# Kernel tuning notes

Hardware: AMD Instinct MI355X
Metric: run time of the kernel (lower is better)

## Reference

```python
import jax, jax.numpy as jnp
import numpy as np

DQ, DM = 1024, 512  # dim_query, dim_mem


def setup_inputs() -> dict:
    key = jax.random.key(0)
    k1, k2, k3, k4, k5, k6 = jax.random.split(key, 6)
    B, S, M = 4, 2048, 4096
    x = jax.random.normal(k1, (B, S, DQ), dtype=jnp.float32)
    memory = jax.random.normal(k2, (B, M, DM), dtype=jnp.float32)
    # nn.Linear params: weight [out, in], bias [out]
    Wq = jax.random.normal(k3, (DM, DQ), dtype=jnp.float32) / np.sqrt(DQ)
    bq = jax.random.normal(k4, (DM,), dtype=jnp.float32) * 0.01
    Wm = jax.random.normal(k5, (DQ, DM), dtype=jnp.float32) / np.sqrt(DM)
    bm = jax.random.normal(k6, (DQ,), dtype=jnp.float32) * 0.01
    return {"x": x, "memory": memory, "Wq": Wq, "bq": bq, "Wm": Wm, "bm": bm}


def reference(x, memory, Wq, bq, Wm, bm):
    # query_transform: [B,S,DQ] -> [B,S,DM]
    query = jnp.einsum('bsq,mq->bsm', x, Wq) + bq
    # unscaled single-head cross-attention over memory slots
    scores = jnp.einsum('bsd,bmd->bsm', query, memory)  # [B,S,M]
    weights = jax.nn.softmax(scores, axis=-1)
    attended = jnp.einsum('bsm,bmd->bsd', weights, memory)  # [B,S,DM]
    # memory_transform: [B,S,DM] -> [B,S,DQ]
    transformed = jnp.einsum('bsd,qd->bsq', attended, Wm) + bm
    return (x, transformed)
```

## Files before the change

kernel.cpp:

```cpp
#include <hip/hip_runtime.h>

typedef unsigned short u16;
typedef __bf16 bf16x8 __attribute__((ext_vector_type(8)));
typedef float f32x4 __attribute__((ext_vector_type(4)));
typedef unsigned short u16x8 __attribute__((ext_vector_type(8)));
typedef unsigned short u16x4 __attribute__((ext_vector_type(4)));

__device__ __forceinline__ u16 f2bf(float f) {
    unsigned u = __builtin_bit_cast(unsigned, f);
    u += 0x7FFFu + ((u >> 16) & 1u);
    return (u16)(u >> 16);
}
__device__ __forceinline__ float bf2f(u16 s) {
    return __builtin_bit_cast(float, ((unsigned)s) << 16);
}

__device__ __forceinline__ void gload16(u16* lds, const u16* g) {
    __builtin_amdgcn_global_load_lds(
        (__attribute__((address_space(1))) unsigned*)g,
        (__attribute__((address_space(3))) unsigned*)lds,
        16, 0, 0);
}

__device__ __forceinline__ void remap_xy(int xcx, int& bx, int& by) {
    const int nx = gridDim.x;
    const int d = blockIdx.y * nx + blockIdx.x;
    const int xcd = d & 7, i = d >> 3;
    const int xcy = 8 / xcx;
    const int cw = nx / xcx;
    const int ch = (int)gridDim.y / xcy;
    bx = (xcd % xcx) * cw + i % cw;
    by = (xcd / xcx) * ch + i / cw;
}

#define BM 128
#define BN 128
#define BK 32
#define TILE (BM * BK)
#define BK2 64
#define TILE2 (BM * BK2)

__device__ __forceinline__ void stage_tile(u16* lds, const u16* src, long long ld,
                                           int k0, int wave, int lane)
{
#pragma unroll
    for (int i = 0; i < 2; ++i) {
        const int segb = wave * 64 + i * 256;
        const int seg  = segb + lane;
        const int r  = seg >> 2;
        const int qs = seg & 3;
        const int qg = qs ^ ((r >> 1) & 3);
        gload16(lds + segb * 8, src + (long long)r * ld + k0 + qg * 8);
    }
}
__device__ __forceinline__ bf16x8 frag(const u16* lds, int row, int quad) {
    const int slot = quad ^ ((row >> 1) & 3);
    return __builtin_bit_cast(bf16x8, *(const u16x8*)(lds + row * BK + slot * 8));
}

__device__ __forceinline__ void stage_tile64(u16* lds, const u16* src, long long ld,
                                             int k0, int wave, int lane)
{
#pragma unroll
    for (int i = 0; i < 4; ++i) {
        const int segb = wave * 64 + i * 256;
        const int seg  = segb + lane;
        const int r  = seg >> 3;
        const int qs = seg & 7;
        const int qg = qs ^ (r & 7);
        gload16(lds + segb * 8, src + (long long)r * ld + k0 + qg * 8);
    }
}
__device__ __forceinline__ bf16x8 frag64(const u16* lds, int row, int quad, int kw) {
    const int slot = (kw * 4 + quad) ^ (row & 7);
    return __builtin_bit_cast(bf16x8, *(const u16x8*)(lds + row * BK2 + slot * 8));
}

#define WAIT8_BARRIER()  asm volatile("s_waitcnt vmcnt(8)\n\ts_barrier" ::: "memory")
#define WAIT0_BARRIER()  asm volatile("s_waitcnt vmcnt(0)\n\ts_barrier" ::: "memory")
#define BARRIER()        asm volatile("s_barrier" ::: "memory")

template<bool SPLITOUT>
__global__ void gemm_cat3(const u16* __restrict__ Ah, const u16* __restrict__ Al,
                          const u16* __restrict__ Bh, const u16* __restrict__ Bl,
                          const float* __restrict__ bias,
                          void* __restrict__ C, u16* __restrict__ Cl,
                          int K, long long lda, long long ldb, long long ldc,
                          int xcx)
{
    __shared__ u16 sm[2][4][TILE];
    const int t = threadIdx.x;
    const int wave = t >> 6, lane = t & 63, quad = lane >> 4, l16 = lane & 15;
    const int waveM = (wave & 1) * 64, waveN = (wave >> 1) * 64;
    int bx, by;
    remap_xy(xcx, bx, by);
    const long long rowBase = (long long)by * BM;
    const long long colBase = (long long)bx * BN;
    Ah += rowBase * lda; Al += rowBase * lda;
    Bh += colBase * ldb; Bl += colBase * ldb;

    f32x4 acc[4][4];
#pragma unroll
    for (int i = 0; i < 4; ++i)
#pragma unroll
        for (int j = 0; j < 4; ++j) acc[i][j] = (f32x4){0.f, 0.f, 0.f, 0.f};

    auto stage4 = [&](int buf, int k0) {
        stage_tile(sm[buf][0], Ah, lda, k0, wave, lane);
        stage_tile(sm[buf][1], Al, lda, k0, wave, lane);
        stage_tile(sm[buf][2], Bh, ldb, k0, wave, lane);
        stage_tile(sm[buf][3], Bl, ldb, k0, wave, lane);
    };

    stage4(0, 0);
    int cur = 0;
    for (int k0 = 0; k0 < K; k0 += BK) {
        if (k0 + BK < K) {
            stage4(cur ^ 1, k0 + BK);
            WAIT8_BARRIER();
        } else {
            WAIT0_BARRIER();
        }

        bf16x8 ah[4], al[4], bh[4], bl[4];
#pragma unroll
        for (int mi = 0; mi < 4; ++mi) {
            int row = waveM + mi * 16 + l16;
            ah[mi] = frag(sm[cur][0], row, quad);
            al[mi] = frag(sm[cur][1], row, quad);
        }
#pragma unroll
        for (int ni = 0; ni < 4; ++ni) {
            int row = waveN + ni * 16 + l16;
            bh[ni] = frag(sm[cur][2], row, quad);
            bl[ni] = frag(sm[cur][3], row, quad);
        }
#pragma unroll
        for (int mi = 0; mi < 4; ++mi)
#pragma unroll
            for (int ni = 0; ni < 4; ++ni) {
                acc[mi][ni] = __builtin_amdgcn_mfma_f32_16x16x32_bf16(al[mi], bh[ni], acc[mi][ni], 0, 0, 0);
                acc[mi][ni] = __builtin_amdgcn_mfma_f32_16x16x32_bf16(ah[mi], bl[ni], acc[mi][ni], 0, 0, 0);
                acc[mi][ni] = __builtin_amdgcn_mfma_f32_16x16x32_bf16(ah[mi], bh[ni], acc[mi][ni], 0, 0, 0);
            }

        BARRIER();
        cur ^= 1;
    }

#pragma unroll
    for (int mi = 0; mi < 4; ++mi) {
#pragma unroll
        for (int ni = 0; ni < 4; ++ni) {
            long long col = colBase + waveN + ni * 16 + l16;
            float bv = bias ? bias[col] : 0.0f;
#pragma unroll
            for (int r = 0; r < 4; ++r) {
                long long row = rowBase + waveM + mi * 16 + quad * 4 + r;
                float f = acc[mi][ni][r] + bv;
                long long off = row * ldc + col;
                if (SPLITOUT) {
                    u16 h = f2bf(f);
                    ((u16*)C)[off] = h;
                    Cl[off] = f2bf(f - bf2f(h));
                } else {
                    ((float*)C)[off] = f;
                }
            }
        }
    }
}

template<bool OUTF32>
__global__ void gemm_bf(const u16* __restrict__ A, const u16* __restrict__ B,
                        const float* __restrict__ bias, void* __restrict__ C,
                        int K, long long lda, long long ldb, long long ldc,
                        int xcx)
{
    __shared__ u16 sm[2][2][TILE2];
    const int t = threadIdx.x;
    const int wave = t >> 6, lane = t & 63, quad = lane >> 4, l16 = lane & 15;
    const int waveM = (wave & 1) * 64, waveN = (wave >> 1) * 64;
    int bx, by;
    remap_xy(xcx, bx, by);
    const long long rowBase = (long long)by * BM;
    const long long colBase = (long long)bx * BN;
    A += rowBase * lda;
    B += colBase * ldb;

    f32x4 acc[4][4];
#pragma unroll
    for (int i = 0; i < 4; ++i)
#pragma unroll
        for (int j = 0; j < 4; ++j) acc[i][j] = (f32x4){0.f, 0.f, 0.f, 0.f};

    auto stage2 = [&](int buf, int k0) {
        stage_tile64(sm[buf][0], A, lda, k0, wave, lane);
        stage_tile64(sm[buf][1], B, ldb, k0, wave, lane);
    };

    stage2(0, 0);
    int cur = 0;
    for (int k0 = 0; k0 < K; k0 += BK2) {
        if (k0 + BK2 < K) {
            stage2(cur ^ 1, k0 + BK2);
            WAIT8_BARRIER();
        } else {
            WAIT0_BARRIER();
        }

#pragma unroll
        for (int kw = 0; kw < 2; ++kw) {
            bf16x8 af[4], bfr[4];
#pragma unroll
            for (int mi = 0; mi < 4; ++mi) af[mi]  = frag64(sm[cur][0], waveM + mi * 16 + l16, quad, kw);
#pragma unroll
            for (int ni = 0; ni < 4; ++ni) bfr[ni] = frag64(sm[cur][1], waveN + ni * 16 + l16, quad, kw);
#pragma unroll
            for (int mi = 0; mi < 4; ++mi)
#pragma unroll
                for (int ni = 0; ni < 4; ++ni)
                    acc[mi][ni] = __builtin_amdgcn_mfma_f32_16x16x32_bf16(af[mi], bfr[ni], acc[mi][ni], 0, 0, 0);
        }

        BARRIER();
        cur ^= 1;
    }

#pragma unroll
    for (int mi = 0; mi < 4; ++mi) {
#pragma unroll
        for (int ni = 0; ni < 4; ++ni) {
            long long col = colBase + waveN + ni * 16 + l16;
            float bv = bias ? bias[col] : 0.0f;
#pragma unroll
            for (int r = 0; r < 4; ++r) {
                long long row = rowBase + waveM + mi * 16 + quad * 4 + r;
                float f = acc[mi][ni][r] + bv;
                long long off = row * ldc + col;
                if (OUTF32) ((float*)C)[off] = f;
                else        ((u16*)C)[off] = f2bf(f);
            }
        }
    }
}

__global__ void gemm_pv(const u16* __restrict__ A, const u16* __restrict__ B,
                        float* __restrict__ part, int KSEG,
                        long long lda, long long ldb)
{
    __shared__ u16 sm[2][2][TILE2];
    const int t = threadIdx.x;
    const int wave = t >> 6, lane = t & 63, quad = lane >> 4, l16 = lane & 15;
    const int waveM = (wave & 1) * 64, waveN = (wave >> 1) * 64;
    const int flat = (blockIdx.z * gridDim.y + blockIdx.y) * gridDim.x + blockIdx.x;
    const int xcd = flat & 7, i = flat >> 3;
    const int by = 2 * xcd + (i & 1);
    const int bx = (i >> 1) & 3;
    const int bz = i >> 3;
    const long long rowBase = (long long)by * BM;
    const long long colBase = (long long)bx * BN;
    const int kbase = bz * KSEG;
    A += rowBase * lda;
    B += colBase * ldb;

    f32x4 acc[4][4];
#pragma unroll
    for (int i2 = 0; i2 < 4; ++i2)
#pragma unroll
        for (int j = 0; j < 4; ++j) acc[i2][j] = (f32x4){0.f, 0.f, 0.f, 0.f};

    auto stage2 = [&](int buf, int k0) {
        stage_tile64(sm[buf][0], A, lda, k0, wave, lane);
        stage_tile64(sm[buf][1], B, ldb, k0, wave, lane);
    };

    stage2(0, kbase);
    int cur = 0;
    for (int k0 = kbase; k0 < kbase + KSEG; k0 += BK2) {
        if (k0 + BK2 < kbase + KSEG) {
            stage2(cur ^ 1, k0 + BK2);
            WAIT8_BARRIER();
        } else {
            WAIT0_BARRIER();
        }

#pragma unroll
        for (int kw = 0; kw < 2; ++kw) {
            bf16x8 af[4], bfr[4];
#pragma unroll
            for (int mi = 0; mi < 4; ++mi) af[mi]  = frag64(sm[cur][0], waveM + mi * 16 + l16, quad, kw);
#pragma unroll
            for (int ni = 0; ni < 4; ++ni) bfr[ni] = frag64(sm[cur][1], waveN + ni * 16 + l16, quad, kw);
#pragma unroll
            for (int mi = 0; mi < 4; ++mi)
#pragma unroll
                for (int ni = 0; ni < 4; ++ni)
                    acc[mi][ni] = __builtin_amdgcn_mfma_f32_16x16x32_bf16(af[mi], bfr[ni], acc[mi][ni], 0, 0, 0);
        }

        BARRIER();
        cur ^= 1;
    }

#pragma unroll
    for (int mi = 0; mi < 4; ++mi) {
#pragma unroll
        for (int ni = 0; ni < 4; ++ni) {
            long long col = colBase + waveN + ni * 16 + l16;
#pragma unroll
            for (int r = 0; r < 4; ++r) {
                long long row = rowBase + waveM + mi * 16 + quad * 4 + r;
                part[row * 4096 + 2048 + bz * 512 + col] = acc[mi][ni][r];
            }
        }
    }
}

__global__ void cvt_att(const float* __restrict__ Sc, u16* __restrict__ dst)
{
    const int row = blockIdx.x, t = threadIdx.x;
    const float* p = Sc + (long long)row * 4096 + 2048 + t * 4;
    float4 s0 = *(const float4*)(p);
    float4 s1 = *(const float4*)(p + 512);
    float4 s2 = *(const float4*)(p + 1024);
    float4 s3 = *(const float4*)(p + 1536);
    u16x4 v;
    v[0] = f2bf(s0.x + s1.x + s2.x + s3.x);
    v[1] = f2bf(s0.y + s1.y + s2.y + s3.y);
    v[2] = f2bf(s0.z + s1.z + s2.z + s3.z);
    v[3] = f2bf(s0.w + s1.w + s2.w + s3.w);
    *(u16x4*)(dst + (long long)row * 512 + t * 4) = v;
}

__global__ void split32(const float* __restrict__ src, u16* __restrict__ h,
                        u16* __restrict__ l, long long n)
{
    long long i = ((long long)blockIdx.x * blockDim.x + threadIdx.x) * 8;
    if (i >= n) return;
    float4 a = *(const float4*)(src + i);
    float4 b = *(const float4*)(src + i + 4);
    float v[8] = {a.x, a.y, a.z, a.w, b.x, b.y, b.z, b.w};
    u16x8 hv, lv;
#pragma unroll
    for (int j = 0; j < 8; ++j) {
        u16 hh = f2bf(v[j]);
        hv[j] = hh;
        lv[j] = f2bf(v[j] - bf2f(hh));
    }
    *(u16x8*)(h + i) = hv;
    *(u16x8*)(l + i) = lv;
}

__global__ void cvt32(const float* __restrict__ src, u16* __restrict__ dst, long long n)
{
    long long i = ((long long)blockIdx.x * blockDim.x + threadIdx.x) * 8;
    if (i >= n) return;
    float4 a = *(const float4*)(src + i);
    float4 b = *(const float4*)(src + i + 4);
    u16x8 v;
    v[0] = f2bf(a.x); v[1] = f2bf(a.y); v[2] = f2bf(a.z); v[3] = f2bf(a.w);
    v[4] = f2bf(b.x); v[5] = f2bf(b.y); v[6] = f2bf(b.z); v[7] = f2bf(b.w);
    *(u16x8*)(dst + i) = v;
}

__global__ void prep_mem(const float* __restrict__ src, u16* __restrict__ h,
                         u16* __restrict__ l, u16* __restrict__ tdst)
{
    __shared__ u16 tile[64][72];
    const int dBase = blockIdx.x * 64, mBase = blockIdx.y * 64;
    const int t = threadIdx.x;
#pragma unroll
    for (int i = 0; i < 4; ++i) {
        int seg = t + i * 256;
        int r = seg >> 4;
        int c = (seg & 15) << 2;
        long long off = (long long)(mBase + r) * 512 + dBase + c;
        float4 v = *(const float4*)(src + off);
        u16 h0 = f2bf(v.x), h1 = f2bf(v.y), h2 = f2bf(v.z), h3 = f2bf(v.w);
        tile[r][c] = h0; tile[r][c + 1] = h1; tile[r][c + 2] = h2; tile[r][c + 3] = h3;
        u16x4 hv; hv[0] = h0; hv[1] = h1; hv[2] = h2; hv[3] = h3;
        u16x4 lv;
        lv[0] = f2bf(v.x - bf2f(h0)); lv[1] = f2bf(v.y - bf2f(h1));
        lv[2] = f2bf(v.z - bf2f(h2)); lv[3] = f2bf(v.w - bf2f(h3));
        *(u16x4*)(h + off) = hv;
        *(u16x4*)(l + off) = lv;
    }
    __syncthreads();
#pragma unroll
    for (int i = 0; i < 2; ++i) {
        int seg = t + i * 256;
        int r = seg >> 3;
        int c = (seg & 7) << 3;
        u16x8 v;
#pragma unroll
        for (int j = 0; j < 8; ++j) v[j] = tile[c + j][r];
        *(u16x8*)(tdst + (long long)(dBase + r) * 4096 + mBase + c) = v;
    }
}

__global__ void softmax_rows(float* __restrict__ S)
{
    const int d = blockIdx.x;
    const int rowIdx = (d & 7) * 256 + (d >> 3);
    float* p = S + (long long)rowIdx * 4096;
    const int t = threadIdx.x;

    float4 v[4];
#pragma unroll
    for (int i = 0; i < 4; ++i) v[i] = ((const float4*)p)[t + i * 256];

    float m = -1e30f;
#pragma unroll
    for (int i = 0; i < 4; ++i)
        m = fmaxf(m, fmaxf(fmaxf(v[i].x, v[i].y), fmaxf(v[i].z, v[i].w)));
#pragma unroll
    for (int off = 32; off; off >>= 1) m = fmaxf(m, __shfl_xor(m, off));
    __shared__ float redm[4];
    if ((t & 63) == 0) redm[t >> 6] = m;
    __syncthreads();
    m = fmaxf(fmaxf(redm[0], redm[1]), fmaxf(redm[2], redm[3]));

    float s = 0.f;
#pragma unroll
    for (int i = 0; i < 4; ++i) {
        v[i].x = __expf(v[i].x - m); v[i].y = __expf(v[i].y - m);
        v[i].z = __expf(v[i].z - m); v[i].w = __expf(v[i].w - m);
        s += v[i].x + v[i].y + v[i].z + v[i].w;
    }
#pragma unroll
    for (int off = 32; off; off >>= 1) s += __shfl_xor(s, off);
    __shared__ float reds[4];
    if ((t & 63) == 0) reds[t >> 6] = s;
    __syncthreads();
    s = reds[0] + reds[1] + reds[2] + reds[3];
    const float inv = 1.0f / s;

    u16* pw = (u16*)p;
#pragma unroll
    for (int i = 0; i < 4; ++i) {
        u16x4 w;
        w[0] = f2bf(v[i].x * inv); w[1] = f2bf(v[i].y * inv);
        w[2] = f2bf(v[i].z * inv); w[3] = f2bf(v[i].w * inv);
        *(u16x4*)(pw + 4 * (t + i * 256)) = w;
    }
}

extern "C" void kernel_launch(void* const* d_in, const int* in_sizes, int n_in,
                              void* d_out, int out_size, void* d_ws, size_t ws_size,
                              hipStream_t stream)
{
    const float* x   = (const float*)d_in[0];
    const float* mem = (const float*)d_in[1];
    const float* Wq  = (const float*)d_in[2];
    const float* bq  = (const float*)d_in[3];
    const float* Wm  = (const float*)d_in[4];
    const float* bm  = (const float*)d_in[5];

    char* base = (char*)d_out;
    u16*   Qh   = (u16*)base;
    u16*   Ql   = (u16*)(base + (8ll  << 20));
    u16*   Mh   = (u16*)(base + (16ll << 20));
    u16*   Ml   = (u16*)(base + (20ll << 20));
    u16*   MemT = (u16*)(base + (24ll << 20));
    u16*   Wqh  = (u16*)(base + (28ll << 20));
    u16*   Wql  = (u16*)(base + (29ll << 20));
    u16*   Wmh  = (u16*)(base + (30ll << 20));
    u16*   Xh   = (u16*)(base + (32ll << 20));
    u16*   Xl   = (u16*)(base + (48ll << 20));
    float* Sc   = (float*)(base + (32ll << 20));
    float* out1 = (float*)d_out + 8388608ll;

    split32<<<4096, 256, 0, stream>>>(x,  Xh,  Xl,  8192ll * 1024);
    split32<<<256,  256, 0, stream>>>(Wq, Wqh, Wql, 512ll * 1024);
    cvt32<<<256,    256, 0, stream>>>(Wm, Wmh,      1024ll * 512);

    gemm_cat3<true><<<dim3(512 / BN, 8192 / BM), 256, 0, stream>>>(
        Xh, Xl, Wqh, Wql, bq, Qh, Ql, 1024, 1024, 1024, 512, 1);

    for (int b = 0; b < 4; ++b) {
        const float* Mb = mem + (long long)b * 4096 * 512;
        u16* Qhb = Qh + (long long)b * 2048 * 512;
        u16* Qlb = Ql + (long long)b * 2048 * 512;

        prep_mem<<<dim3(8, 64), 256, 0, stream>>>(Mb, Mh, Ml, MemT);

        gemm_cat3<false><<<dim3(4096 / BN, 2048 / BM), 256, 0, stream>>>(
            Qhb, Qlb, Mh, Ml, nullptr, Sc, nullptr, 512, 512, 512, 4096, 4);

        softmax_rows<<<dim3(2048), 256, 0, stream>>>(Sc);

        gemm_pv<<<dim3(512 / BN, 2048 / BM, 4), 256, 0, stream>>>(
            (const u16*)Sc, MemT, Sc, 1024, 8192, 4096);

        cvt_att<<<dim3(2048), 128, 0, stream>>>(Sc, Qhb);
    }

    gemm_bf<true><<<dim3(1024 / BN, 8192 / BM), 256, 0, stream>>>(
        Qh, Wmh, bm, out1, 512, 512, 512, 1024, 1);

    hipMemcpyAsync(d_out, x, 8192ll * 1024 * 4, hipMemcpyDeviceToDevice, stream);
}
```

Before: 451.4 us.

## Batch attention kernels across all four batches using a workspace buffer

Replaces the per-batch loop of five kernel launches with single batched launches that cover all four batches via blockIdx.z or a decoded batch index. Each batch gets its own memory-split and score buffers in a large workspace. This cuts launch count and serialization, and gives the small per-batch grids more blocks to fill the GPU. It needs at least 176 MB of workspace and falls back to the old loop otherwise.

```diff
diff --git a/kernel.cpp b/kernel.cpp
--- a/kernel.cpp
+++ b/kernel.cpp
@@ -86,12 +86,17 @@
                           const float* __restrict__ bias,
                           void* __restrict__ C, u16* __restrict__ Cl,
                           int K, long long lda, long long ldb, long long ldc,
-                          int xcx)
+                          int xcx, long long abstride, long long bbstride,
+                          long long cbstride)
 {
     __shared__ u16 sm[2][4][TILE];
     const int t = threadIdx.x;
     const int wave = t >> 6, lane = t & 63, quad = lane >> 4, l16 = lane & 15;
     const int waveM = (wave & 1) * 64, waveN = (wave >> 1) * 64;
+    const int batch = blockIdx.z;
+    Ah += batch * abstride; Al += batch * abstride;
+    Bh += batch * bbstride; Bl += batch * bbstride;
+    void* Cb = SPLITOUT ? C : (void*)((float*)C + (long long)batch * cbstride);
     int bx, by;
     remap_xy(xcx, bx, by);
     const long long rowBase = (long long)by * BM;
@@ -161,10 +166,10 @@
                 long long off = row * ldc + col;
                 if (SPLITOUT) {
                     u16 h = f2bf(f);
-                    ((u16*)C)[off] = h;
+                    ((u16*)Cb)[off] = h;
                     Cl[off] = f2bf(f - bf2f(h));
                 } else {
-                    ((float*)C)[off] = f;
+                    ((float*)Cb)[off] = f;
                 }
             }
         }
@@ -247,7 +252,8 @@
 
 __global__ void gemm_pv(const u16* __restrict__ A, const u16* __restrict__ B,
                         float* __restrict__ part, int KSEG,
-                        long long lda, long long ldb)
+                        long long lda, long long ldb,
+                        long long abstride, long long bbstride, long long pbstride)
 {
     __shared__ u16 sm[2][2][TILE2];
     const int t = threadIdx.x;
@@ -255,9 +261,12 @@
     const int waveM = (wave & 1) * 64, waveN = (wave >> 1) * 64;
     const int flat = (blockIdx.z * gridDim.y + blockIdx.y) * gridDim.x + blockIdx.x;
     const int xcd = flat & 7, i = flat >> 3;
-    const int by = 2 * xcd + (i & 1);
-    const int bx = (i >> 1) & 3;
-    const int bz = i >> 3;
+    const int batch = i >> 5;
+    const int j = i & 31;
+    const int by = 2 * xcd + (j & 1);
+    const int bx = (j >> 1) & 3;
+    const int bz = j >> 3;
+    A += batch * abstride; B += batch * bbstride; part += batch * pbstride;
     const long long rowBase = (long long)by * BM;
     const long long colBase = (long long)bx * BN;
     const int kbase = bz * KSEG;
@@ -268,7 +277,7 @@
 #pragma unroll
     for (int i2 = 0; i2 < 4; ++i2)
 #pragma unroll
-        for (int j = 0; j < 4; ++j) acc[i2][j] = (f32x4){0.f, 0.f, 0.f, 0.f};
+        for (int j2 = 0; j2 < 4; ++j2) acc[i2][j2] = (f32x4){0.f, 0.f, 0.f, 0.f};
 
     auto stage2 = [&](int buf, int k0) {
         stage_tile64(sm[buf][0], A, lda, k0, wave, lane);
@@ -317,10 +326,12 @@
     }
 }
 
-__global__ void cvt_att(const float* __restrict__ Sc, u16* __restrict__ dst)
-{
-    const int row = blockIdx.x, t = threadIdx.x;
-    const float* p = Sc + (long long)row * 4096 + 2048 + t * 4;
+__global__ void cvt_att(const float* __restrict__ Sc, u16* __restrict__ dst,
+                        long long sbstride, long long dbstride)
+{
+    const int d = blockIdx.x, t = threadIdx.x;
+    const int batch = d >> 11, row = d & 2047;
+    const float* p = Sc + (long long)batch * sbstride + (long long)row * 4096 + 2048 + t * 4;
     float4 s0 = *(const float4*)(p);
     float4 s1 = *(const float4*)(p + 512);
     float4 s2 = *(const float4*)(p + 1024);
@@ -330,7 +341,7 @@
     v[1] = f2bf(s0.y + s1.y + s2.y + s3.y);
     v[2] = f2bf(s0.z + s1.z + s2.z + s3.z);
     v[3] = f2bf(s0.w + s1.w + s2.w + s3.w);
-    *(u16x4*)(dst + (long long)row * 512 + t * 4) = v;
+    *(u16x4*)(dst + (long long)batch * dbstride + (long long)row * 512 + t * 4) = v;
 }
 
 __global__ void split32(const float* __restrict__ src, u16* __restrict__ h,
@@ -365,9 +376,13 @@
 }
 
 __global__ void prep_mem(const float* __restrict__ src, u16* __restrict__ h,
-                         u16* __restrict__ l, u16* __restrict__ tdst)
+                         u16* __restrict__ l, u16* __restrict__ tdst,
+                         long long sstride, long long mstride, long long tstride)
 {
     __shared__ u16 tile[64][72];
+    const int batch = blockIdx.z;
+    src += batch * sstride; h += batch * mstride; l += batch * mstride;
+    tdst += batch * tstride;
     const int dBase = blockIdx.x * 64, mBase = blockIdx.y * 64;
     const int t = threadIdx.x;
 #pragma unroll
@@ -399,11 +414,12 @@
     }
 }
 
-__global__ void softmax_rows(float* __restrict__ S)
+__global__ void softmax_rows(float* __restrict__ S, long long bstride)
 {
     const int d = blockIdx.x;
-    const int rowIdx = (d & 7) * 256 + (d >> 3);
-    float* p = S + (long long)rowIdx * 4096;
+    const int local = d & 2047, batch = d >> 11;
+    const int rowIdx = (local & 7) * 256 + (local >> 3);
+    float* p = S + (long long)batch * bstride + (long long)rowIdx * 4096;
     const int t = threadIdx.x;
 
     float4 v[4];
@@ -475,28 +491,55 @@
     split32<<<256,  256, 0, stream>>>(Wq, Wqh, Wql, 512ll * 1024);
     cvt32<<<256,    256, 0, stream>>>(Wm, Wmh,      1024ll * 512);
 
-    gemm_cat3<true><<<dim3(512 / BN, 8192 / BM), 256, 0, stream>>>(
-        Xh, Xl, Wqh, Wql, bq, Qh, Ql, 1024, 1024, 1024, 512, 1);
-
-    for (int b = 0; b < 4; ++b) {
-        const float* Mb = mem + (long long)b * 4096 * 512;
-        u16* Qhb = Qh + (long long)b * 2048 * 512;
-        u16* Qlb = Ql + (long long)b * 2048 * 512;
-
-        prep_mem<<<dim3(8, 64), 256, 0, stream>>>(Mb, Mh, Ml, MemT);
-
-        gemm_cat3<false><<<dim3(4096 / BN, 2048 / BM), 256, 0, stream>>>(
-            Qhb, Qlb, Mh, Ml, nullptr, Sc, nullptr, 512, 512, 512, 4096, 4);
-
-        softmax_rows<<<dim3(2048), 256, 0, stream>>>(Sc);
-
-        gemm_pv<<<dim3(512 / BN, 2048 / BM, 4), 256, 0, stream>>>(
-            (const u16*)Sc, MemT, Sc, 1024, 8192, 4096);
-
-        cvt_att<<<dim3(2048), 128, 0, stream>>>(Sc, Qhb);
-    }
-
-    gemm_bf<true><<<dim3(1024 / BN, 8192 / BM), 256, 0, stream>>>(
+    gemm_cat3<true><<<dim3(512 / BN, 8192 / BM, 1), 256, 0, stream>>>(
+        Xh, Xl, Wqh, Wql, bq, Qh, Ql, 1024, 1024, 1024, 512, 1, 0, 0, 0);
+
+    const bool big_ws = (d_ws != nullptr) && (ws_size >= (176ull << 20));
+    if (big_ws) {
+        char* wsb = (char*)d_ws;
+        u16*   Mh4 = (u16*)wsb;
+        u16*   Ml4 = (u16*)(wsb + (16ll << 20));
+        u16*   MT4 = (u16*)(wsb + (32ll << 20));
+        float* Sc4 = (float*)(wsb + (48ll << 20));
+
+        prep_mem<<<dim3(8, 64, 4), 256, 0, stream>>>(
+            mem, Mh4, Ml4, MT4, 4096ll * 512, 4096ll * 512, 512ll * 4096);
+
+        gemm_cat3<false><<<dim3(4096 / BN, 2048 / BM, 4), 256, 0, stream>>>(
+            Qh, Ql, Mh4, Ml4, nullptr, Sc4, nullptr, 512, 512, 512, 4096, 4,
+            2048ll * 512, 4096ll * 512, 2048ll * 4096);
+
+        softmax_rows<<<dim3(8192), 256, 0, stream>>>(Sc4, 2048ll * 4096);
+
+        gemm_pv<<<dim3(4, 16, 16), 256, 0, stream>>>(
+            (const u16*)Sc4, MT4, Sc4, 1024, 8192, 4096,
+            2048ll * 8192, 512ll * 4096, 2048ll * 4096);
+
+        cvt_att<<<dim3(8192), 128, 0, stream>>>(
+            Sc4, Qh, 2048ll * 4096, 2048ll * 512);
+    } else {
+        for (int b = 0; b < 4; ++b) {
+            const float* Mb = mem + (long long)b * 4096 * 512;
+            u16* Qhb = Qh + (long long)b * 2048 * 512;
+            u16* Qlb = Ql + (long long)b * 2048 * 512;
+
+            prep_mem<<<dim3(8, 64, 1), 256, 0, stream>>>(
+                Mb, Mh, Ml, MemT, 0, 0, 0);
+
+            gemm_cat3<false><<<dim3(4096 / BN, 2048 / BM, 1), 256, 0, stream>>>(
+                Qhb, Qlb, Mh, Ml, nullptr, Sc, nullptr, 512, 512, 512, 4096, 4,
+                0, 0, 0);
+
+            softmax_rows<<<dim3(2048), 256, 0, stream>>>(Sc, 0);
+
+            gemm_pv<<<dim3(4, 16, 4), 256, 0, stream>>>(
+                (const u16*)Sc, MemT, Sc, 1024, 8192, 4096, 0, 0, 0);
+
+            cvt_att<<<dim3(2048), 128, 0, stream>>>(Sc, Qhb, 0, 0);
+        }
+    }
+
+    gemm_bf<true><<<dim3(1024 / BN, 8192 / BM, 1), 256, 0, stream>>>(
         Qh, Wmh, bm, out1, 512, 512, 512, 1024, 1);
 
     hipMemcpyAsync(d_out, x, 8192ll * 1024 * 4, hipMemcpyDeviceToDevice, stream);
```

New measurement: 388.3 us. 14.0% less time.
